# Kernel optimization log

Measured on AMD Instinct MI355X. Metric: run time of the kernel, lower is better.

The kernel has to match this reference:

```python
import jax, jax.numpy as jnp
import numpy as np

WORKSPACE_RADIUS = 1.0
WORKSPACE_HEIGHT = 1.0


def setup_inputs() -> dict:
    key = jax.random.key(0)
    k1, k2 = jax.random.split(key)
    # (B, N, 6): xyz + normals, already padded to common length N
    pointclouds = jax.random.normal(k1, (32, 131072, 6), dtype=jnp.float32)
    # (B, 4, 4): homogeneous task transforms
    task_transform = jax.random.normal(k2, (32, 4, 4), dtype=jnp.float32)
    return {"pointclouds": pointclouds, "task_transform": task_transform}


def reference(pointclouds, task_transform):
    # Split xyz points and normals
    pts = pointclouds[..., :3]          # (B, N, 3)
    nrm = pointclouds[..., 3:]          # (B, N, 3)

    rot = task_transform[:, :3, :3]     # (B, 3, 3)
    trans = task_transform[:, :3, 3]    # (B, 3)

    # points @ rotation + translation (matches torch.matmul(points, rotation))
    p = jnp.einsum('bnd,bde->bne', pts, rot) + trans[:, None, :]

    # padded rows have all-zero normals
    non_padded = jnp.sum(nrm, axis=-1) != 0

    sq_dist = p[..., 0] ** 2 + p[..., 1] ** 2
    in_range = (sq_dist < WORKSPACE_RADIUS ** 2) & (p[..., 2] < WORKSPACE_HEIGHT)
    valid = in_range & non_padded      # (B, N)

    # Filter-and-repad: compact valid points to the front (stable = order
    # preserving, as in the torch boolean-index version), zero the tail.
    order = jnp.argsort(~valid, axis=1, stable=True)                 # (B, N)
    gathered = jnp.take_along_axis(pointclouds, order[..., None], axis=1)
    mask_sorted = jnp.take_along_axis(valid, order, axis=1)
    return gathered * mask_sorted[..., None].astype(pointclouds.dtype)
```

## Files before the change

kernel.cpp:

```cpp
#include <hip/hip_runtime.h>
#include <cstdint>

namespace {

constexpr int kB   = 32;
constexpr int kN   = 131072;
constexpr int kC   = 6;
constexpr int TPB  = 256;
constexpr int BPB  = kN / TPB;
constexpr int NBLK = kB * BPB;
constexpr int WAVES = TPB / 64;

__device__ __forceinline__ bool point_valid(const float* __restrict__ pc,
                                            const float* __restrict__ tt,
                                            int b, int n,
                                            float2& a0, float2& a1, float2& a2) {
    const float* T = tt + b * 16;
    const float2* row = (const float2*)(pc + ((size_t)b * kN + n) * kC);
    a0 = row[0];
    a1 = row[1];
    a2 = row[2];
    const float x = a0.x, y = a0.y, z = a1.x;
    const float nsum = (a1.y + a2.x) + a2.y;
    const float px = x * T[0] + y * T[4] + z * T[8]  + T[3];
    const float py = x * T[1] + y * T[5] + z * T[9]  + T[7];
    const float pz = x * T[2] + y * T[6] + z * T[10] + T[11];
    return (px * px + py * py < 1.0f) && (pz < 1.0f) && (nsum != 0.0f);
}

__global__ __launch_bounds__(TPB) void k_count(const float* __restrict__ pc,
                                               const float* __restrict__ tt,
                                               uint64_t* __restrict__ masks,
                                               int* __restrict__ blkCnt,
                                               int writeMask) {
    const int blk = blockIdx.x;
    const int b   = blk / BPB;
    const int k   = blk - b * BPB;
    const int tid = threadIdx.x;
    const int n   = k * TPB + tid;

    float2 a0, a1, a2;
    const bool valid = point_valid(pc, tt, b, n, a0, a1, a2);
    const uint64_t m = __ballot(valid);

    const int lane = tid & 63;
    const int wv   = tid >> 6;
    __shared__ int wc[WAVES];
    if (lane == 0) {
        if (writeMask) masks[(size_t)blk * WAVES + wv] = m;
        wc[wv] = __popcll(m);
    }
    __syncthreads();
    if (tid == 0) blkCnt[blk] = wc[0] + wc[1] + wc[2] + wc[3];
}

__global__ __launch_bounds__(BPB) void k_scan(const int* __restrict__ blkCnt,
                                              int* __restrict__ blkPre,
                                              int* __restrict__ batchTot) {
    const int b = blockIdx.x;
    const int t = threadIdx.x;
    __shared__ int s[BPB];
    const int v = blkCnt[b * BPB + t];
    s[t] = v;
    __syncthreads();
    for (int off = 1; off < BPB; off <<= 1) {
        int u = (t >= off) ? s[t - off] : 0;
        __syncthreads();
        s[t] += u;
        __syncthreads();
    }
    blkPre[b * BPB + t] = s[t] - v;
    if (t == BPB - 1) batchTot[b] = s[t];
}

template <bool USE_MASK>
__global__ __launch_bounds__(TPB) void k_scatter(const float* __restrict__ pc,
                                                 const float* __restrict__ tt,
                                                 const uint64_t* __restrict__ masks,
                                                 const int* __restrict__ blkPre,
                                                 const int* __restrict__ batchTot,
                                                 float* __restrict__ out) {
    const int blk = blockIdx.x;
    const int b   = blk / BPB;
    const int k   = blk - b * BPB;
    const int tid = threadIdx.x;
    const int n   = k * TPB + tid;
    const int lane = tid & 63;
    const int wv   = tid >> 6;

    uint64_t m;
    float2 a0, a1, a2;
    bool valid;
    if (USE_MASK) {
        m = masks[(size_t)blk * WAVES + wv];
        valid = (m >> lane) & 1ull;
    } else {
        valid = point_valid(pc, tt, b, n, a0, a1, a2);
        m = __ballot(valid);
    }

    __shared__ int wc[WAVES];
    if (lane == 0) wc[wv] = __popcll(m);
    __syncthreads();
    int waveBase = 0;
#pragma unroll
    for (int w = 0; w < WAVES - 1; ++w)
        if (w < wv) waveBase += wc[w];

    const int base   = blkPre[blk] + waveBase;
    const int before = __popcll(m & ((1ull << lane) - 1ull));
    const int vcnt   = base + before;
    const size_t outB = (size_t)b * kN;

    if (valid) {
        if (USE_MASK) {
            const float2* row = (const float2*)(pc + (outB + (size_t)n) * kC);
            a0 = row[0]; a1 = row[1]; a2 = row[2];
        }
        float2* o = (float2*)(out + (outB + (size_t)vcnt) * kC);
        o[0] = a0; o[1] = a1; o[2] = a2;
    } else {
        const int invRank = n - vcnt;
        const int dst = batchTot[b] + invRank;
        float2* o = (float2*)(out + (outB + (size_t)dst) * kC);
        const float2 zz = make_float2(0.0f, 0.0f);
        o[0] = zz; o[1] = zz; o[2] = zz;
    }
}

}

extern "C" void kernel_launch(void* const* d_in, const int* in_sizes, int n_in,
                              void* d_out, int out_size, void* d_ws, size_t ws_size,
                              hipStream_t stream) {
    const float* pc = (const float*)d_in[0];
    const float* tt = (const float*)d_in[1];
    float* out = (float*)d_out;

    const size_t maskBytes = (size_t)NBLK * WAVES * sizeof(uint64_t);
    const size_t intBytes  = (size_t)(2 * NBLK + kB) * sizeof(int);
    const bool useMask = ws_size >= (maskBytes + intBytes);

    uint64_t* masks;
    int *blkCnt, *blkPre, *batchTot;
    if (useMask) {
        masks    = (uint64_t*)d_ws;
        blkCnt   = (int*)((char*)d_ws + maskBytes);
    } else {
        masks    = nullptr;
        blkCnt   = (int*)d_ws;
    }
    blkPre   = blkCnt + NBLK;
    batchTot = blkPre + NBLK;

    k_count<<<NBLK, TPB, 0, stream>>>(pc, tt, masks, blkCnt, useMask ? 1 : 0);
    k_scan<<<kB, BPB, 0, stream>>>(blkCnt, blkPre, batchTot);
    if (useMask) {
        k_scatter<true><<<NBLK, TPB, 0, stream>>>(pc, tt, masks, blkPre, batchTot, out);
    } else {
        k_scatter<false><<<NBLK, TPB, 0, stream>>>(pc, tt, nullptr, blkPre, batchTot, out);
    }
}
```

Before: 44.80 us.

## Fold block-prefix scan into scatter kernel and stage count loads through LDS

Removes the separate per-batch scan kernel: each scatter block now reads all 512 block counts of its batch and computes its own exclusive prefix and batch total with wave shuffles. This drops one launch and its serialization. The cost is that every block redundantly reads 2 KB of counts. The count kernel also loads its tile with coalesced float4 reads into shared memory instead of strided float2 row reads, and the mask path is now always used.

```diff
diff --git a/kernel.cpp b/kernel.cpp
--- a/kernel.cpp
+++ b/kernel.cpp
@@ -11,117 +11,95 @@
 constexpr int NBLK = kB * BPB;
 constexpr int WAVES = TPB / 64;
 
-__device__ __forceinline__ bool point_valid(const float* __restrict__ pc,
-                                            const float* __restrict__ tt,
-                                            int b, int n,
-                                            float2& a0, float2& a1, float2& a2) {
-    const float* T = tt + b * 16;
-    const float2* row = (const float2*)(pc + ((size_t)b * kN + n) * kC);
-    a0 = row[0];
-    a1 = row[1];
-    a2 = row[2];
-    const float x = a0.x, y = a0.y, z = a1.x;
-    const float nsum = (a1.y + a2.x) + a2.y;
-    const float px = x * T[0] + y * T[4] + z * T[8]  + T[3];
-    const float py = x * T[1] + y * T[5] + z * T[9]  + T[7];
-    const float pz = x * T[2] + y * T[6] + z * T[10] + T[11];
-    return (px * px + py * py < 1.0f) && (pz < 1.0f) && (nsum != 0.0f);
+__device__ __forceinline__ int waveSum(int v) {
+#pragma unroll
+    for (int off = 32; off; off >>= 1) v += __shfl_xor(v, off, 64);
+    return v;
 }
 
 __global__ __launch_bounds__(TPB) void k_count(const float* __restrict__ pc,
                                                const float* __restrict__ tt,
                                                uint64_t* __restrict__ masks,
-                                               int* __restrict__ blkCnt,
-                                               int writeMask) {
+                                               int* __restrict__ blkCnt) {
     const int blk = blockIdx.x;
-    const int b   = blk / BPB;
-    const int k   = blk - b * BPB;
+    const int b   = blk >> 9;
+    const int k   = blk & (BPB - 1);
     const int tid = threadIdx.x;
-    const int n   = k * TPB + tid;
-
-    float2 a0, a1, a2;
-    const bool valid = point_valid(pc, tt, b, n, a0, a1, a2);
-    const uint64_t m = __ballot(valid);
-
     const int lane = tid & 63;
     const int wv   = tid >> 6;
+
+    __shared__ float4 sbuf[384];
+    const float4* src = (const float4*)(pc + ((size_t)b * kN + (size_t)k * TPB) * kC);
+    sbuf[tid] = src[tid];
+    if (tid < 128) sbuf[256 + tid] = src[256 + tid];
+    __syncthreads();
+
+    const float* r = (const float*)sbuf + tid * 6;
+    const float x = r[0], y = r[1], z = r[2];
+    const float nsum = (r[3] + r[4]) + r[5];
+
+    const float* T = tt + b * 16;
+    const float px = x * T[0] + y * T[4] + z * T[8]  + T[3];
+    const float py = x * T[1] + y * T[5] + z * T[9]  + T[7];
+    const float pz = x * T[2] + y * T[6] + z * T[10] + T[11];
+    const bool valid = (px * px + py * py < 1.0f) && (pz < 1.0f) && (nsum != 0.0f);
+
+    const uint64_t m = __ballot(valid);
     __shared__ int wc[WAVES];
     if (lane == 0) {
-        if (writeMask) masks[(size_t)blk * WAVES + wv] = m;
+        masks[(size_t)blk * WAVES + wv] = m;
         wc[wv] = __popcll(m);
     }
     __syncthreads();
     if (tid == 0) blkCnt[blk] = wc[0] + wc[1] + wc[2] + wc[3];
 }
 
-__global__ __launch_bounds__(BPB) void k_scan(const int* __restrict__ blkCnt,
-                                              int* __restrict__ blkPre,
-                                              int* __restrict__ batchTot) {
-    const int b = blockIdx.x;
-    const int t = threadIdx.x;
-    __shared__ int s[BPB];
-    const int v = blkCnt[b * BPB + t];
-    s[t] = v;
-    __syncthreads();
-    for (int off = 1; off < BPB; off <<= 1) {
-        int u = (t >= off) ? s[t - off] : 0;
-        __syncthreads();
-        s[t] += u;
-        __syncthreads();
-    }
-    blkPre[b * BPB + t] = s[t] - v;
-    if (t == BPB - 1) batchTot[b] = s[t];
-}
-
-template <bool USE_MASK>
 __global__ __launch_bounds__(TPB) void k_scatter(const float* __restrict__ pc,
-                                                 const float* __restrict__ tt,
                                                  const uint64_t* __restrict__ masks,
-                                                 const int* __restrict__ blkPre,
-                                                 const int* __restrict__ batchTot,
+                                                 const int* __restrict__ blkCnt,
                                                  float* __restrict__ out) {
     const int blk = blockIdx.x;
-    const int b   = blk / BPB;
-    const int k   = blk - b * BPB;
+    const int b   = blk >> 9;
+    const int k   = blk & (BPB - 1);
     const int tid = threadIdx.x;
     const int n   = k * TPB + tid;
     const int lane = tid & 63;
     const int wv   = tid >> 6;
 
-    uint64_t m;
-    float2 a0, a1, a2;
-    bool valid;
-    if (USE_MASK) {
-        m = masks[(size_t)blk * WAVES + wv];
-        valid = (m >> lane) & 1ull;
-    } else {
-        valid = point_valid(pc, tt, b, n, a0, a1, a2);
-        m = __ballot(valid);
-    }
+    __shared__ int wc[WAVES];
+    __shared__ int pw[WAVES], tw[WAVES];
 
-    __shared__ int wc[WAVES];
+    const uint64_t m = masks[(size_t)blk * WAVES + wv];
+    const bool valid = (m >> lane) & 1ull;
     if (lane == 0) wc[wv] = __popcll(m);
+
+    const int* cnt = blkCnt + b * BPB;
+    const int c0 = cnt[tid];
+    const int c1 = cnt[tid + 256];
+    int myPref = (tid < k ? c0 : 0) + (tid + 256 < k ? c1 : 0);
+    int myTot  = c0 + c1;
+    const int prefW = waveSum(myPref);
+    const int totW  = waveSum(myTot);
+    if (lane == 0) { pw[wv] = prefW; tw[wv] = totW; }
     __syncthreads();
+    const int prefix = (pw[0] + pw[1]) + (pw[2] + pw[3]);
+    const int total  = (tw[0] + tw[1]) + (tw[2] + tw[3]);
+
     int waveBase = 0;
 #pragma unroll
     for (int w = 0; w < WAVES - 1; ++w)
         if (w < wv) waveBase += wc[w];
-
-    const int base   = blkPre[blk] + waveBase;
     const int before = __popcll(m & ((1ull << lane) - 1ull));
-    const int vcnt   = base + before;
+    const int vcnt   = prefix + waveBase + before;
     const size_t outB = (size_t)b * kN;
 
     if (valid) {
-        if (USE_MASK) {
-            const float2* row = (const float2*)(pc + (outB + (size_t)n) * kC);
-            a0 = row[0]; a1 = row[1]; a2 = row[2];
-        }
+        const float2* row = (const float2*)(pc + (outB + (size_t)n) * kC);
+        const float2 a0 = row[0], a1 = row[1], a2 = row[2];
         float2* o = (float2*)(out + (outB + (size_t)vcnt) * kC);
         o[0] = a0; o[1] = a1; o[2] = a2;
     } else {
-        const int invRank = n - vcnt;
-        const int dst = batchTot[b] + invRank;
+        const int dst = total + (n - vcnt);
         float2* o = (float2*)(out + (outB + (size_t)dst) * kC);
         const float2 zz = make_float2(0.0f, 0.0f);
         o[0] = zz; o[1] = zz; o[2] = zz;
@@ -137,27 +115,9 @@
     const float* tt = (const float*)d_in[1];
     float* out = (float*)d_out;
 
-    const size_t maskBytes = (size_t)NBLK * WAVES * sizeof(uint64_t);
-    const size_t intBytes  = (size_t)(2 * NBLK + kB) * sizeof(int);
-    const bool useMask = ws_size >= (maskBytes + intBytes);
+    int* blkCnt      = (int*)d_ws;
+    uint64_t* masks  = (uint64_t*)((char*)d_ws + (size_t)NBLK * sizeof(int));
 
-    uint64_t* masks;
-    int *blkCnt, *blkPre, *batchTot;
-    if (useMask) {
-        masks    = (uint64_t*)d_ws;
-        blkCnt   = (int*)((char*)d_ws + maskBytes);
-    } else {
-        masks    = nullptr;
-        blkCnt   = (int*)d_ws;
-    }
-    blkPre   = blkCnt + NBLK;
-    batchTot = blkPre + NBLK;
-
-    k_count<<<NBLK, TPB, 0, stream>>>(pc, tt, masks, blkCnt, useMask ? 1 : 0);
-    k_scan<<<kB, BPB, 0, stream>>>(blkCnt, blkPre, batchTot);
-    if (useMask) {
-        k_scatter<true><<<NBLK, TPB, 0, stream>>>(pc, tt, masks, blkPre, batchTot, out);
-    } else {
-        k_scatter<false><<<NBLK, TPB, 0, stream>>>(pc, tt, nullptr, blkPre, batchTot, out);
-    }
+    k_count<<<NBLK, TPB, 0, stream>>>(pc, tt, masks, blkCnt);
+    k_scatter<<<NBLK, TPB, 0, stream>>>(pc, masks, blkCnt, out);
 }
```

Result: slower. 47.33 us (+5.6%).
